# Kernel optimization log

Measured on AMD Instinct MI355X. Metric: run time of the kernel, lower is better.

Reference implementation:

```python
import jax, jax.numpy as jnp
import numpy as np

DIM = 512
HEADS = 8
HEAD_DIM = DIM // HEADS
MLP_HIDDEN = int(DIM * 4.0)
B, N = 4, 2048
LS_INIT = 1e-5
EPS = 1e-5


def _layernorm(x, w, b):
    mu = jnp.mean(x, axis=-1, keepdims=True)
    var = jnp.mean(jnp.square(x - mu), axis=-1, keepdims=True)
    return (x - mu) * jax.lax.rsqrt(var + EPS) * w + b


def setup_inputs() -> dict:
    key = jax.random.key(0)
    ks = jax.random.split(key, 12)
    s = 0.02
    return {
        "x": jax.random.normal(ks[0], (B, N, DIM), jnp.float32),
        "rel_pos_bias": jax.random.normal(ks[1], (HEADS, N, N), jnp.float32),
        "qkv_w": jax.random.normal(ks[2], (DIM, 3 * DIM), jnp.float32) * s,
        "qkv_b": jnp.zeros((3 * DIM,), jnp.float32),
        "out_w": jax.random.normal(ks[3], (DIM, DIM), jnp.float32) * s,
        "out_b": jnp.zeros((DIM,), jnp.float32),
        "ln1_w": jnp.ones((DIM,), jnp.float32),
        "ln1_b": jnp.zeros((DIM,), jnp.float32),
        "ln2_w": jnp.ones((DIM,), jnp.float32),
        "ln2_b": jnp.zeros((DIM,), jnp.float32),
        "ffn_w1": jax.random.normal(ks[4], (DIM, MLP_HIDDEN), jnp.float32) * s,
        "ffn_b1": jnp.zeros((MLP_HIDDEN,), jnp.float32),
        "ffn_w2": jax.random.normal(ks[5], (MLP_HIDDEN, DIM), jnp.float32) * s,
        "ffn_b2": jnp.zeros((DIM,), jnp.float32),
        "gamma1": jnp.full((DIM,), LS_INIT, jnp.float32),
        "gamma2": jnp.full((DIM,), LS_INIT, jnp.float32),
    }


def reference(x, rel_pos_bias, qkv_w, qkv_b, out_w, out_b, ln1_w, ln1_b,
              ln2_w, ln2_b, ffn_w1, ffn_b1, ffn_w2, ffn_b2, gamma1, gamma2):
    # Pre-norm MHA with relative-position bias
    y = _layernorm(x, ln1_w, ln1_b)                       # [B,N,C]
    qkv = y @ qkv_w + qkv_b                               # [B,N,3C]
    qkv = qkv.reshape(B, N, 3, HEADS, HEAD_DIM)
    q = jnp.transpose(qkv[:, :, 0], (0, 2, 1, 3))         # [B,H,N,D]
    k = jnp.transpose(qkv[:, :, 1], (0, 2, 1, 3))
    v = jnp.transpose(qkv[:, :, 2], (0, 2, 1, 3))
    scale = 1.0 / np.sqrt(HEAD_DIM).astype(np.float32)
    attn = jnp.einsum("bhid,bhjd->bhij", q, k) * scale    # [B,H,N,N]
    attn = attn + rel_pos_bias[None]
    attn = jax.nn.softmax(attn, axis=-1)
    out = jnp.einsum("bhij,bhjd->bhid", attn, v)          # [B,H,N,D]
    out = jnp.transpose(out, (0, 2, 1, 3)).reshape(B, N, DIM)
    out = out @ out_w + out_b
    x = x + out * gamma1                                  # layer scale, no drop-path (eval)
    # FFN with exact GELU
    y2 = _layernorm(x, ln2_w, ln2_b)
    h = jax.nn.gelu(y2 @ ffn_w1 + ffn_b1, approximate=False)
    ffn_out = h @ ffn_w2 + ffn_b2
    x = x + ffn_out * gamma2
    return x
```

## Files before the change

kernel.cpp:

```cpp
#include <hip/hip_runtime.h>
#include <hip/hip_bf16.h>
#include <math.h>

#define SEQ 2048
#define BATCH 4
#define DM 512
#define NH 8
#define HD 64
#define HID 2048
#define ROWS (BATCH * SEQ)

typedef __attribute__((ext_vector_type(8))) short short8;
typedef __attribute__((ext_vector_type(4))) float f32x4;

__device__ __forceinline__ short f2bf(float f) {
    unsigned u = __float_as_uint(f);
    u += 0x7fff + ((u >> 16) & 1);
    return (short)(u >> 16);
}

__device__ __forceinline__ void gl2lds16(const void* g, void* l) {
    __builtin_amdgcn_global_load_lds(
        (const __attribute__((address_space(1))) void*)g,
        (__attribute__((address_space(3))) void*)l, 16, 0, 0);
}

__global__ __launch_bounds__(256) void tcast_k(const float* __restrict__ W,
                                               short* __restrict__ Wt,
                                               int K, int N) {
    __shared__ float tile[32][33];
    int tx = threadIdx.x, ty = threadIdx.y;
    int n0 = blockIdx.x * 32, k0 = blockIdx.y * 32;
#pragma unroll
    for (int i = 0; i < 4; ++i)
        tile[ty + i * 8][tx] = W[(size_t)(k0 + ty + i * 8) * N + n0 + tx];
    __syncthreads();
#pragma unroll
    for (int i = 0; i < 4; ++i)
        Wt[(size_t)(n0 + ty + i * 8) * K + k0 + tx] = f2bf(tile[tx][ty + i * 8]);
}

__global__ __launch_bounds__(256) void ln_k(const float* __restrict__ X,
                                            const float* __restrict__ g,
                                            const float* __restrict__ bta,
                                            short* __restrict__ Y) {
    int t = threadIdx.x;
    int wv = t >> 6, ln = t & 63;
    size_t row = (size_t)blockIdx.x * 4 + wv;
    const float* xr = X + row * DM;
    float4 v0 = *(const float4*)(xr + ln * 4);
    float4 v1 = *(const float4*)(xr + 256 + ln * 4);
    float s = v0.x + v0.y + v0.z + v0.w + v1.x + v1.y + v1.z + v1.w;
    float q = v0.x * v0.x + v0.y * v0.y + v0.z * v0.z + v0.w * v0.w +
              v1.x * v1.x + v1.y * v1.y + v1.z * v1.z + v1.w * v1.w;
#pragma unroll
    for (int off = 1; off < 64; off <<= 1) {
        s += __shfl_xor(s, off);
        q += __shfl_xor(q, off);
    }
    float mean = s * (1.0f / 512.0f);
    float var = q * (1.0f / 512.0f) - mean * mean;
    float rstd = rsqrtf(var + 1e-5f);
    int c0 = ln * 4, c1 = 256 + ln * 4;
    ushort4 o0, o1;
    o0.x = (unsigned short)f2bf((v0.x - mean) * rstd * g[c0 + 0] + bta[c0 + 0]);
    o0.y = (unsigned short)f2bf((v0.y - mean) * rstd * g[c0 + 1] + bta[c0 + 1]);
    o0.z = (unsigned short)f2bf((v0.z - mean) * rstd * g[c0 + 2] + bta[c0 + 2]);
    o0.w = (unsigned short)f2bf((v0.w - mean) * rstd * g[c0 + 3] + bta[c0 + 3]);
    o1.x = (unsigned short)f2bf((v1.x - mean) * rstd * g[c1 + 0] + bta[c1 + 0]);
    o1.y = (unsigned short)f2bf((v1.y - mean) * rstd * g[c1 + 1] + bta[c1 + 1]);
    o1.z = (unsigned short)f2bf((v1.z - mean) * rstd * g[c1 + 2] + bta[c1 + 2]);
    o1.w = (unsigned short)f2bf((v1.w - mean) * rstd * g[c1 + 3] + bta[c1 + 3]);
    *(ushort4*)((unsigned short*)Y + row * DM + c0) = o0;
    *(ushort4*)((unsigned short*)Y + row * DM + c1) = o1;
}

template <int EPI, int TN>
__global__ __launch_bounds__(256) void gemm_bt(const short* __restrict__ A,
                                               const short* __restrict__ Bt,
                                               const float* __restrict__ bias,
                                               const float* __restrict__ gamma,
                                               const float* __restrict__ res,
                                               void* __restrict__ Cout,
                                               short* __restrict__ Cout2,
                                               int M, int N, int K) {
    constexpr int NI = TN / 32;
    __shared__ __attribute__((aligned(16))) short As[128][32];
    __shared__ __attribute__((aligned(16))) short Bs[TN][32];
    int t = threadIdx.x;
    int w = t >> 6, ln = t & 63;
    int quad = ln >> 4, l15 = ln & 15;
    int n0 = blockIdx.x * TN, m0 = blockIdx.y * 128;
    int wm = (w & 1) * 64, wn = (w >> 1) * (TN / 2);

    int srow0 = w * 32 + (ln >> 2);
    int srow1 = srow0 + 16;
    int srowB = w * 16 + (ln >> 2);
    int schunk = (ln & 3) * 8;
    const short* Ag0 = A + (size_t)(m0 + srow0) * K + schunk;
    const short* Ag1 = A + (size_t)(m0 + srow1) * K + schunk;

    f32x4 acc[4][NI];
#pragma unroll
    for (int i = 0; i < 4; ++i)
#pragma unroll
        for (int j = 0; j < NI; ++j) acc[i][j] = (f32x4){0.f, 0.f, 0.f, 0.f};

    for (int k0 = 0; k0 < K; k0 += 32) {
        __syncthreads();
        gl2lds16(Ag0 + k0, &As[srow0][schunk]);
        gl2lds16(Ag1 + k0, &As[srow1][schunk]);
        if (TN == 128) {
            gl2lds16(Bt + (size_t)(n0 + srow0) * K + k0 + schunk, &Bs[srow0 & (TN - 1)][schunk]);
            gl2lds16(Bt + (size_t)(n0 + srow1) * K + k0 + schunk, &Bs[srow1 & (TN - 1)][schunk]);
        } else {
            gl2lds16(Bt + (size_t)(n0 + srowB) * K + k0 + schunk, &Bs[srowB & (TN - 1)][schunk]);
        }
        __syncthreads();
        short8 af[4], bf[NI];
#pragma unroll
        for (int mi = 0; mi < 4; ++mi)
            af[mi] = *(const short8*)&As[wm + mi * 16 + l15][quad * 8];
#pragma unroll
        for (int ni = 0; ni < NI; ++ni)
            bf[ni] = *(const short8*)&Bs[wn + ni * 16 + l15][quad * 8];
#pragma unroll
        for (int mi = 0; mi < 4; ++mi)
#pragma unroll
            for (int ni = 0; ni < NI; ++ni)
                acc[mi][ni] = __builtin_amdgcn_mfma_f32_16x16x32_bf16(
                    af[mi], bf[ni], acc[mi][ni], 0, 0, 0);
    }

    if (EPI == 3 && n0 >= 1024) {
#pragma unroll
        for (int mi = 0; mi < 4; ++mi) {
#pragma unroll
            for (int ni = 0; ni < NI; ++ni) {
                int col = n0 + wn + ni * 16 + l15;
                int d = col - 1024, hh = d >> 6, dd = d & 63;
                int row0 = m0 + wm + mi * 16 + quad * 4;
                int bb = row0 >> 11, key = row0 & 2047;
                float bs = bias[col];
                ushort4 pk;
                pk.x = (unsigned short)f2bf(acc[mi][ni][0] + bs);
                pk.y = (unsigned short)f2bf(acc[mi][ni][1] + bs);
                pk.z = (unsigned short)f2bf(acc[mi][ni][2] + bs);
                pk.w = (unsigned short)f2bf(acc[mi][ni][3] + bs);
                *(ushort4*)&Cout2[((size_t)(bb * 8 + hh) * 64 + dd) * 2048 + key] = pk;
            }
        }
    } else {
#pragma unroll
        for (int mi = 0; mi < 4; ++mi) {
#pragma unroll
            for (int ni = 0; ni < NI; ++ni) {
#pragma unroll
                for (int r = 0; r < 4; ++r) {
                    int row = m0 + wm + mi * 16 + quad * 4 + r;
                    int col = n0 + wn + ni * 16 + l15;
                    float v = acc[mi][ni][r] + bias[col];
                    if (EPI == 0) {
                        ((short*)Cout)[(size_t)row * N + col] = f2bf(v);
                    } else if (EPI == 1) {
                        float gg = 0.5f * v * (1.0f + erff(v * 0.70710678118654752f));
                        ((short*)Cout)[(size_t)row * N + col] = f2bf(gg);
                    } else if (EPI == 2) {
                        ((float*)Cout)[(size_t)row * N + col] =
                            fmaf(v, gamma[col], res[(size_t)row * N + col]);
                    } else {
                        float sc = (n0 < 512) ? 0.18033688f : 1.0f;
                        ((short*)Cout)[(size_t)row * 1024 + col] = f2bf(v * sc);
                    }
                }
            }
        }
    }
}

__global__ __launch_bounds__(256, 4) void attn_k(const short* __restrict__ qkv,
                                                 const short* __restrict__ vT,
                                                 const float* __restrict__ bias,
                                                 short* __restrict__ Aout) {
    __shared__ __attribute__((aligned(16))) short Ks[64 * 64];
    __shared__ __attribute__((aligned(16))) short Vs[64 * 64];
    __shared__ __attribute__((aligned(16))) float Bsf[64 * 64];
    __shared__ __attribute__((aligned(16))) short Ps[4][16 * 64];
    int t = threadIdx.x;
    int w = t >> 6, ln = t & 63, quad = ln >> 4, l15 = ln & 15;
    int idx = blockIdx.x;
    int h = idx & 7, b = (idx >> 3) & 3, qt = idx >> 5;
    int qb = qt * 64 + w * 16;
    const size_t cbase = (size_t)b * SEQ * 1024;

    const short* qrow = qkv + cbase + (size_t)(qb + l15) * 1024 + h * 64;
    short8 qf0 = *(const short8*)(qrow + quad * 8);
    short8 qf1 = *(const short8*)(qrow + 32 + quad * 8);

    int kr = t >> 3, kc = t & 7;
    const short* kg = qkv + cbase + 512 + h * 64 + kc * 8;
    const short* vg = vT + ((size_t)(b * 8 + h) * 64) * 2048 + kc * 8;
    int bq = t >> 2, bc = t & 3;
    const float* bg = bias + (size_t)h * SEQ * SEQ + (size_t)(qt * 64 + bq) * SEQ + bc * 4;

    int kswz = ((kc ^ (kr & 7)) * 8);
    int kd0 = kr * 64 + kswz;
    int kd1 = kd0 + 32 * 64;
    int bofs[4];
#pragma unroll
    for (int r = 0; r < 4; ++r)
        bofs[r] = bq * 64 + (((r * 4 + bc) ^ (bq & 15)) * 4);

    short8 ones;
#pragma unroll
    for (int i = 0; i < 8; ++i) ones[i] = (short)0x3F80;

    f32x4 o[4], ol;
#pragma unroll
    for (int db = 0; db < 4; ++db) o[db] = (f32x4){0.f, 0.f, 0.f, 0.f};
    ol = (f32x4){0.f, 0.f, 0.f, 0.f};

    int sw7 = l15 & 7;

    float4 pk0 = *(const float4*)(kg + (size_t)kr * 1024);
    float4 pk1 = *(const float4*)(kg + (size_t)(kr + 32) * 1024);
    float4 pv0 = *(const float4*)(vg + (size_t)kr * 2048);
    float4 pv1 = *(const float4*)(vg + (size_t)(kr + 32) * 2048);
    float4 pb0 = *(const float4*)(bg + 0);
    float4 pb1 = *(const float4*)(bg + 16);
    float4 pb2 = *(const float4*)(bg + 32);
    float4 pb3 = *(const float4*)(bg + 48);

    for (int jt = 0; jt < 32; ++jt) {
        __syncthreads();
        *(float4*)&Ks[kd0] = pk0;
        *(float4*)&Ks[kd1] = pk1;
        *(float4*)&Vs[kd0] = pv0;
        *(float4*)&Vs[kd1] = pv1;
        *(float4*)&Bsf[bofs[0]] = pb0;
        *(float4*)&Bsf[bofs[1]] = pb1;
        *(float4*)&Bsf[bofs[2]] = pb2;
        *(float4*)&Bsf[bofs[3]] = pb3;
        __syncthreads();
        int j1 = (jt < 31) ? (jt + 1) * 64 : jt * 64;
        pk0 = *(const float4*)(kg + (size_t)(j1 + kr) * 1024);
        pk1 = *(const float4*)(kg + (size_t)(j1 + kr + 32) * 1024);
        pv0 = *(const float4*)(vg + (size_t)kr * 2048 + j1);
        pv1 = *(const float4*)(vg + (size_t)(kr + 32) * 2048 + j1);
        pb0 = *(const float4*)(bg + j1);
        pb1 = *(const float4*)(bg + j1 + 16);
        pb2 = *(const float4*)(bg + j1 + 32);
        pb3 = *(const float4*)(bg + j1 + 48);

        f32x4 s4[4];
#pragma unroll
        for (int ni = 0; ni < 4; ++ni) {
            short8 k0 = *(const short8*)&Ks[(ni * 16 + l15) * 64 + ((quad ^ sw7) * 8)];
            short8 k1 = *(const short8*)&Ks[(ni * 16 + l15) * 64 + (((4 + quad) ^ sw7) * 8)];
            s4[ni] = (f32x4){0.f, 0.f, 0.f, 0.f};
            s4[ni] = __builtin_amdgcn_mfma_f32_16x16x32_bf16(k0, qf0, s4[ni], 0, 0, 0);
            s4[ni] = __builtin_amdgcn_mfma_f32_16x16x32_bf16(k1, qf1, s4[ni], 0, 0, 0);
        }
#pragma unroll
        for (int ni = 0; ni < 4; ++ni) {
            float4 bb = *(const float4*)&Bsf[(w * 16 + l15) * 64 + (((ni * 4 + quad) ^ l15) * 4)];
            float2 plo, phi;
            plo.x = exp2f(fmaf(bb.x, 1.44269504f, s4[ni][0]));
            plo.y = exp2f(fmaf(bb.y, 1.44269504f, s4[ni][1]));
            phi.x = exp2f(fmaf(bb.z, 1.44269504f, s4[ni][2]));
            phi.y = exp2f(fmaf(bb.w, 1.44269504f, s4[ni][3]));
            __hip_bfloat162 l2 = __float22bfloat162_rn(plo);
            __hip_bfloat162 h2 = __float22bfloat162_rn(phi);
            union { uint2 u; } pp;
            pp.u.x = *(unsigned*)&l2;
            pp.u.y = *(unsigned*)&h2;
            int c = ni * 2 + (quad >> 1);
            *(uint2*)&Ps[w][l15 * 64 + ((c ^ sw7) * 8) + (quad & 1) * 4] = pp.u;
        }
#pragma unroll
        for (int kk = 0; kk < 2; ++kk) {
            short8 ap = *(const short8*)&Ps[w][l15 * 64 + (((kk * 4 + quad) ^ sw7) * 8)];
#pragma unroll
            for (int db = 0; db < 4; ++db) {
                short8 vv = *(const short8*)&Vs[(db * 16 + l15) * 64 + (((kk * 4 + quad) ^ sw7) * 8)];
                o[db] = __builtin_amdgcn_mfma_f32_16x16x32_bf16(ap, vv, o[db], 0, 0, 0);
            }
            ol = __builtin_amdgcn_mfma_f32_16x16x32_bf16(ap, ones, ol, 0, 0, 0);
        }
    }
#pragma unroll
    for (int r = 0; r < 4; ++r) {
        float inv = 1.0f / ol[r];
        int qrow_g = b * SEQ + qb + quad * 4 + r;
#pragma unroll
        for (int db = 0; db < 4; ++db) {
            Aout[(size_t)qrow_g * DM + h * 64 + db * 16 + l15] =
                f2bf(o[db][r] * inv);
        }
    }
}

extern "C" void kernel_launch(void* const* d_in, const int* in_sizes, int n_in,
                              void* d_out, int out_size, void* d_ws, size_t ws_size,
                              hipStream_t stream) {
    const float* x      = (const float*)d_in[0];
    const float* bias   = (const float*)d_in[1];
    const float* qkv_w  = (const float*)d_in[2];
    const float* qkv_b  = (const float*)d_in[3];
    const float* out_w  = (const float*)d_in[4];
    const float* out_b  = (const float*)d_in[5];
    const float* ln1_w  = (const float*)d_in[6];
    const float* ln1_b  = (const float*)d_in[7];
    const float* ln2_w  = (const float*)d_in[8];
    const float* ln2_b  = (const float*)d_in[9];
    const float* ffn_w1 = (const float*)d_in[10];
    const float* ffn_b1 = (const float*)d_in[11];
    const float* ffn_w2 = (const float*)d_in[12];
    const float* ffn_b2 = (const float*)d_in[13];
    const float* gamma1 = (const float*)d_in[14];
    const float* gamma2 = (const float*)d_in[15];
    float* out = (float*)d_out;

    short* wqkvT = (short*)d_ws;
    short* woutT = wqkvT + (size_t)1536 * 512;
    short* w1T   = woutT + (size_t)512 * 512;
    short* w2T   = w1T + (size_t)2048 * 512;
    short* y1    = w2T + (size_t)512 * 2048;
    short* qkvB  = y1 + (size_t)ROWS * DM;
    short* vTb   = qkvB + (size_t)ROWS * 1024;
    short* aoutB = vTb + (size_t)32 * 64 * 2048;
    float* x1    = (float*)(aoutB + (size_t)ROWS * DM);
    short* hB    = qkvB;

    tcast_k<<<dim3(1536 / 32, 512 / 32), dim3(32, 8), 0, stream>>>(qkv_w, wqkvT, 512, 1536);
    tcast_k<<<dim3(512 / 32, 512 / 32), dim3(32, 8), 0, stream>>>(out_w, woutT, 512, 512);
    tcast_k<<<dim3(2048 / 32, 512 / 32), dim3(32, 8), 0, stream>>>(ffn_w1, w1T, 512, 2048);
    tcast_k<<<dim3(512 / 32, 2048 / 32), dim3(32, 8), 0, stream>>>(ffn_w2, w2T, 2048, 512);

    ln_k<<<ROWS / 4, 256, 0, stream>>>(x, ln1_w, ln1_b, y1);
    gemm_bt<3, 128><<<dim3(1536 / 128, ROWS / 128), 256, 0, stream>>>(
        y1, wqkvT, qkv_b, nullptr, nullptr, qkvB, vTb, ROWS, 1536, 512);
    attn_k<<<1024, 256, 0, stream>>>(qkvB, vTb, bias, aoutB);
    gemm_bt<2, 64><<<dim3(512 / 64, ROWS / 128), 256, 0, stream>>>(
        aoutB, woutT, out_b, gamma1, x, x1, nullptr, ROWS, 512, 512);
    ln_k<<<ROWS / 4, 256, 0, stream>>>(x1, ln2_w, ln2_b, y1);
    gemm_bt<1, 128><<<dim3(2048 / 128, ROWS / 128), 256, 0, stream>>>(
        y1, w1T, ffn_b1, nullptr, nullptr, hB, nullptr, ROWS, 2048, 512);
    gemm_bt<2, 64><<<dim3(512 / 64, ROWS / 128), 256, 0, stream>>>(
        hB, w2T, ffn_b2, gamma2, x1, out, nullptr, ROWS, 512, 2048);
}
```

Baseline: 446.9 us.

## Merge weight casts, double K-step in GEMM, load attention bias directly, approximate GELU

Four weight-transpose/cast launches are merged into one kernel with block-index dispatch. The GEMM main loop now loads two 32-wide K slices per sync, halving barrier count at the cost of doubled LDS. The attention kernel drops the LDS staging of the relative-position bias and prefetches each lane's bias fragment straight into registers. The exact erf GELU is replaced by a tanh-style sigmoid approximation, which changes numerics relative to the exact-GELU reference.

```diff
diff --git a/kernel.cpp b/kernel.cpp
--- a/kernel.cpp
+++ b/kernel.cpp
@@ -25,19 +25,28 @@
         (__attribute__((address_space(3))) void*)l, 16, 0, 0);
 }
 
-__global__ __launch_bounds__(256) void tcast_k(const float* __restrict__ W,
-                                               short* __restrict__ Wt,
-                                               int K, int N) {
+__global__ __launch_bounds__(256) void tcast_all(
+    const float* __restrict__ qkv_w, const float* __restrict__ out_w,
+    const float* __restrict__ w1, const float* __restrict__ w2,
+    short* __restrict__ o_qkv, short* __restrict__ o_out,
+    short* __restrict__ o_w1, short* __restrict__ o_w2) {
     __shared__ float tile[32][33];
+    int id = blockIdx.x;
+    const float* W; short* O; int K, N;
+    if (id < 768)       { W = qkv_w; O = o_qkv; K = 512;  N = 1536; }
+    else if (id < 1024) { W = out_w; O = o_out; K = 512;  N = 512;  id -= 768; }
+    else if (id < 2048) { W = w1;    O = o_w1;  K = 512;  N = 2048; id -= 1024; }
+    else                { W = w2;    O = o_w2;  K = 2048; N = 512;  id -= 2048; }
+    int tn = N / 32;
+    int n0 = (id % tn) * 32, k0 = (id / tn) * 32;
     int tx = threadIdx.x, ty = threadIdx.y;
-    int n0 = blockIdx.x * 32, k0 = blockIdx.y * 32;
 #pragma unroll
     for (int i = 0; i < 4; ++i)
         tile[ty + i * 8][tx] = W[(size_t)(k0 + ty + i * 8) * N + n0 + tx];
     __syncthreads();
 #pragma unroll
     for (int i = 0; i < 4; ++i)
-        Wt[(size_t)(n0 + ty + i * 8) * K + k0 + tx] = f2bf(tile[tx][ty + i * 8]);
+        O[(size_t)(n0 + ty + i * 8) * K + k0 + tx] = f2bf(tile[tx][ty + i * 8]);
 }
 
 __global__ __launch_bounds__(256) void ln_k(const float* __restrict__ X,
@@ -85,8 +94,10 @@
                                                short* __restrict__ Cout2,
                                                int M, int N, int K) {
     constexpr int NI = TN / 32;
-    __shared__ __attribute__((aligned(16))) short As[128][32];
-    __shared__ __attribute__((aligned(16))) short Bs[TN][32];
+    __shared__ __attribute__((aligned(16))) short As0[128][32];
+    __shared__ __attribute__((aligned(16))) short As1[128][32];
+    __shared__ __attribute__((aligned(16))) short Bs0[TN][32];
+    __shared__ __attribute__((aligned(16))) short Bs1[TN][32];
     int t = threadIdx.x;
     int w = t >> 6, ln = t & 63;
     int quad = ln >> 4, l15 = ln & 15;
@@ -99,6 +110,9 @@
     int schunk = (ln & 3) * 8;
     const short* Ag0 = A + (size_t)(m0 + srow0) * K + schunk;
     const short* Ag1 = A + (size_t)(m0 + srow1) * K + schunk;
+    const short* Bg0 = Bt + (size_t)(n0 + srow0) * K + schunk;
+    const short* Bg1 = Bt + (size_t)(n0 + srow1) * K + schunk;
+    const short* BgB = Bt + (size_t)(n0 + srowB) * K + schunk;
 
     f32x4 acc[4][NI];
 #pragma unroll
@@ -106,30 +120,52 @@
 #pragma unroll
         for (int j = 0; j < NI; ++j) acc[i][j] = (f32x4){0.f, 0.f, 0.f, 0.f};
 
-    for (int k0 = 0; k0 < K; k0 += 32) {
+    for (int k0 = 0; k0 < K; k0 += 64) {
         __syncthreads();
-        gl2lds16(Ag0 + k0, &As[srow0][schunk]);
-        gl2lds16(Ag1 + k0, &As[srow1][schunk]);
+        gl2lds16(Ag0 + k0, &As0[srow0][schunk]);
+        gl2lds16(Ag1 + k0, &As0[srow1][schunk]);
+        gl2lds16(Ag0 + k0 + 32, &As1[srow0][schunk]);
+        gl2lds16(Ag1 + k0 + 32, &As1[srow1][schunk]);
         if (TN == 128) {
-            gl2lds16(Bt + (size_t)(n0 + srow0) * K + k0 + schunk, &Bs[srow0 & (TN - 1)][schunk]);
-            gl2lds16(Bt + (size_t)(n0 + srow1) * K + k0 + schunk, &Bs[srow1 & (TN - 1)][schunk]);
+            gl2lds16(Bg0 + k0, &Bs0[srow0 & (TN - 1)][schunk]);
+            gl2lds16(Bg1 + k0, &Bs0[srow1 & (TN - 1)][schunk]);
+            gl2lds16(Bg0 + k0 + 32, &Bs1[srow0 & (TN - 1)][schunk]);
+            gl2lds16(Bg1 + k0 + 32, &Bs1[srow1 & (TN - 1)][schunk]);
         } else {
-            gl2lds16(Bt + (size_t)(n0 + srowB) * K + k0 + schunk, &Bs[srowB & (TN - 1)][schunk]);
+            gl2lds16(BgB + k0, &Bs0[srowB & (TN - 1)][schunk]);
+            gl2lds16(BgB + k0 + 32, &Bs1[srowB & (TN - 1)][schunk]);
         }
         __syncthreads();
-        short8 af[4], bf[NI];
-#pragma unroll
-        for (int mi = 0; mi < 4; ++mi)
-            af[mi] = *(const short8*)&As[wm + mi * 16 + l15][quad * 8];
-#pragma unroll
-        for (int ni = 0; ni < NI; ++ni)
-            bf[ni] = *(const short8*)&Bs[wn + ni * 16 + l15][quad * 8];
-#pragma unroll
-        for (int mi = 0; mi < 4; ++mi)
+        {
+            short8 af[4], bf[NI];
+#pragma unroll
+            for (int mi = 0; mi < 4; ++mi)
+                af[mi] = *(const short8*)&As0[wm + mi * 16 + l15][quad * 8];
 #pragma unroll
             for (int ni = 0; ni < NI; ++ni)
-                acc[mi][ni] = __builtin_amdgcn_mfma_f32_16x16x32_bf16(
-                    af[mi], bf[ni], acc[mi][ni], 0, 0, 0);
+                bf[ni] = *(const short8*)&Bs0[wn + ni * 16 + l15][quad * 8];
+#pragma unroll
+            for (int mi = 0; mi < 4; ++mi)
+#pragma unroll
+                for (int ni = 0; ni < NI; ++ni)
+                    acc[mi][ni] = __builtin_amdgcn_mfma_f32_16x16x32_bf16(
+                        af[mi], bf[ni], acc[mi][ni], 0, 0, 0);
+        }
+        {
+            short8 af[4], bf[NI];
+#pragma unroll
+            for (int mi = 0; mi < 4; ++mi)
+                af[mi] = *(const short8*)&As1[wm + mi * 16 + l15][quad * 8];
+#pragma unroll
+            for (int ni = 0; ni < NI; ++ni)
+                bf[ni] = *(const short8*)&Bs1[wn + ni * 16 + l15][quad * 8];
+#pragma unroll
+            for (int mi = 0; mi < 4; ++mi)
+#pragma unroll
+                for (int ni = 0; ni < NI; ++ni)
+                    acc[mi][ni] = __builtin_amdgcn_mfma_f32_16x16x32_bf16(
+                        af[mi], bf[ni], acc[mi][ni], 0, 0, 0);
+        }
     }
 
     if (EPI == 3 && n0 >= 1024) {
@@ -163,7 +199,8 @@
                     if (EPI == 0) {
                         ((short*)Cout)[(size_t)row * N + col] = f2bf(v);
                     } else if (EPI == 1) {
-                        float gg = 0.5f * v * (1.0f + erff(v * 0.70710678118654752f));
+                        float u = v * fmaf(v * v, 0.0713548162f, 1.59576912f);
+                        float gg = v / (1.0f + __expf(-u));
                         ((short*)Cout)[(size_t)row * N + col] = f2bf(gg);
                     } else if (EPI == 2) {
                         ((float*)Cout)[(size_t)row * N + col] =
@@ -184,7 +221,6 @@
                                                  short* __restrict__ Aout) {
     __shared__ __attribute__((aligned(16))) short Ks[64 * 64];
     __shared__ __attribute__((aligned(16))) short Vs[64 * 64];
-    __shared__ __attribute__((aligned(16))) float Bsf[64 * 64];
     __shared__ __attribute__((aligned(16))) short Ps[4][16 * 64];
     int t = threadIdx.x;
     int w = t >> 6, ln = t & 63, quad = ln >> 4, l15 = ln & 15;
@@ -200,16 +236,12 @@
     int kr = t >> 3, kc = t & 7;
     const short* kg = qkv + cbase + 512 + h * 64 + kc * 8;
     const short* vg = vT + ((size_t)(b * 8 + h) * 64) * 2048 + kc * 8;
-    int bq = t >> 2, bc = t & 3;
-    const float* bg = bias + (size_t)h * SEQ * SEQ + (size_t)(qt * 64 + bq) * SEQ + bc * 4;
-
     int kswz = ((kc ^ (kr & 7)) * 8);
     int kd0 = kr * 64 + kswz;
     int kd1 = kd0 + 32 * 64;
-    int bofs[4];
-#pragma unroll
-    for (int r = 0; r < 4; ++r)
-        bofs[r] = bq * 64 + (((r * 4 + bc) ^ (bq & 15)) * 4);
+
+    const float* bias_q = bias + (size_t)h * SEQ * SEQ +
+                          (size_t)(qb + l15) * SEQ + quad * 4;
 
     short8 ones;
 #pragma unroll
@@ -226,10 +258,10 @@
     float4 pk1 = *(const float4*)(kg + (size_t)(kr + 32) * 1024);
     float4 pv0 = *(const float4*)(vg + (size_t)kr * 2048);
     float4 pv1 = *(const float4*)(vg + (size_t)(kr + 32) * 2048);
-    float4 pb0 = *(const float4*)(bg + 0);
-    float4 pb1 = *(const float4*)(bg + 16);
-    float4 pb2 = *(const float4*)(bg + 32);
-    float4 pb3 = *(const float4*)(bg + 48);
+    float4 bbc[4];
+#pragma unroll
+    for (int ni = 0; ni < 4; ++ni)
+        bbc[ni] = *(const float4*)(bias_q + ni * 16);
 
     for (int jt = 0; jt < 32; ++jt) {
         __syncthreads();
@@ -237,20 +269,12 @@
         *(float4*)&Ks[kd1] = pk1;
         *(float4*)&Vs[kd0] = pv0;
         *(float4*)&Vs[kd1] = pv1;
-        *(float4*)&Bsf[bofs[0]] = pb0;
-        *(float4*)&Bsf[bofs[1]] = pb1;
-        *(float4*)&Bsf[bofs[2]] = pb2;
-        *(float4*)&Bsf[bofs[3]] = pb3;
         __syncthreads();
         int j1 = (jt < 31) ? (jt + 1) * 64 : jt * 64;
         pk0 = *(const float4*)(kg + (size_t)(j1 + kr) * 1024);
         pk1 = *(const float4*)(kg + (size_t)(j1 + kr + 32) * 1024);
         pv0 = *(const float4*)(vg + (size_t)kr * 2048 + j1);
         pv1 = *(const float4*)(vg + (size_t)(kr + 32) * 2048 + j1);
-        pb0 = *(const float4*)(bg + j1);
-        pb1 = *(const float4*)(bg + j1 + 16);
-        pb2 = *(const float4*)(bg + j1 + 32);
-        pb3 = *(const float4*)(bg + j1 + 48);
 
         f32x4 s4[4];
 #pragma unroll
@@ -263,12 +287,13 @@
         }
 #pragma unroll
         for (int ni = 0; ni < 4; ++ni) {
-            float4 bb = *(const float4*)&Bsf[(w * 16 + l15) * 64 + (((ni * 4 + quad) ^ l15) * 4)];
+            float4 bb = bbc[ni];
             float2 plo, phi;
             plo.x = exp2f(fmaf(bb.x, 1.44269504f, s4[ni][0]));
             plo.y = exp2f(fmaf(bb.y, 1.44269504f, s4[ni][1]));
             phi.x = exp2f(fmaf(bb.z, 1.44269504f, s4[ni][2]));
             phi.y = exp2f(fmaf(bb.w, 1.44269504f, s4[ni][3]));
+            bbc[ni] = *(const float4*)(bias_q + j1 + ni * 16);
             __hip_bfloat162 l2 = __float22bfloat162_rn(plo);
             __hip_bfloat162 h2 = __float22bfloat162_rn(phi);
             union { uint2 u; } pp;
@@ -332,11 +357,8 @@
     float* x1    = (float*)(aoutB + (size_t)ROWS * DM);
     short* hB    = qkvB;
 
-    tcast_k<<<dim3(1536 / 32, 512 / 32), dim3(32, 8), 0, stream>>>(qkv_w, wqkvT, 512, 1536);
-    tcast_k<<<dim3(512 / 32, 512 / 32), dim3(32, 8), 0, stream>>>(out_w, woutT, 512, 512);
-    tcast_k<<<dim3(2048 / 32, 512 / 32), dim3(32, 8), 0, stream>>>(ffn_w1, w1T, 512, 2048);
-    tcast_k<<<dim3(512 / 32, 2048 / 32), dim3(32, 8), 0, stream>>>(ffn_w2, w2T, 2048, 512);
-
+    tcast_all<<<3072, dim3(32, 8), 0, stream>>>(qkv_w, out_w, ffn_w1, ffn_w2,
+                                                wqkvT, woutT, w1T, w2T);
     ln_k<<<ROWS / 4, 256, 0, stream>>>(x, ln1_w, ln1_b, y1);
     gemm_bt<3, 128><<<dim3(1536 / 128, ROWS / 128), 256, 0, stream>>>(
         y1, wqkvT, qkv_b, nullptr, nullptr, qkvB, vTb, ROWS, 1536, 512);
```

Result: no change. 441.9 us (-1.1%).
